# Kernel tuning notes

Hardware: AMD Instinct MI355X
Metric: run time of the kernel (lower is better)

## Reference

```python
import jax, jax.numpy as jnp
import numpy as np

HID, H, HKV, D, INT, S, T = 2048, 16, 8, 128, 6144, 4096, 512
POS = 0          # absolute position of the first token in this prefill chunk
EPS = 1e-6
SCALE = 1.0 / D ** 0.5
REP = H // HKV


def setup_inputs() -> dict:
    key = jax.random.key(0)
    ks = jax.random.split(key, 12)
    w = lambda k, sh: jax.random.normal(k, sh, dtype=jnp.float32) * 0.02

    hidden_conv = jax.random.normal(ks[0], (1, HID, 1, T), dtype=jnp.float32)

    # RoPE tables for absolute positions POS..POS+T-1, HF half-rotation layout
    inv_freq = 1.0 / (10000.0 ** (jnp.arange(0, D, 2, dtype=jnp.float32) / D))
    pos = (POS + jnp.arange(T, dtype=jnp.float32))
    ang = pos[:, None] * inv_freq[None, :]                      # (T, D/2)
    emb = jnp.concatenate([ang, ang], axis=-1)                  # (T, D)
    cos = jnp.cos(emb)[None]                                    # (1, T, D)
    sin = jnp.sin(emb)[None]

    # one-hot write mask: column t has a 1 at row POS+t
    update_mask = jnp.zeros((S, T), jnp.float32).at[POS + jnp.arange(T), jnp.arange(T)].set(1.0)[None, None]
    # causal mask over the cache: slot s visible to token t iff s <= POS+t
    attn_mask = jnp.where(jnp.arange(S)[None, :] <= (POS + jnp.arange(T))[:, None], 0.0, -1e4).astype(jnp.float32)[None, None]

    k_cache = jnp.zeros((1, HKV, S, D), jnp.float32)
    v_cache = jnp.zeros((1, HKV, S, D), jnp.float32)

    return dict(
        hidden_conv=hidden_conv, cos=cos, sin=sin,
        update_mask=update_mask, attn_mask=attn_mask,
        k_cache=k_cache, v_cache=v_cache,
        wq=w(ks[1], (H * D, HID)), wk=w(ks[2], (HKV * D, HID)),
        wv=w(ks[3], (HKV * D, HID)), wo=w(ks[4], (HID, H * D)),
        ln1_w=jnp.ones((HID,), jnp.float32), ln2_w=jnp.ones((HID,), jnp.float32),
        qn_w=jnp.ones((D,), jnp.float32), kn_w=jnp.ones((D,), jnp.float32),
        w_gate_up=w(ks[5], (2 * INT, HID)), w_down=w(ks[6], (HID, INT)),
    )


def _rms(x, w):
    return x * jax.lax.rsqrt(jnp.mean(x * x, axis=-1, keepdims=True) + EPS) * w


def _rotate_half(x):
    x1, x2 = jnp.split(x, 2, axis=-1)
    return jnp.concatenate([-x2, x1], axis=-1)


def reference(hidden_conv, cos, sin, update_mask, attn_mask, k_cache, v_cache,
              wq, wk, wv, wo, ln1_w, ln2_w, qn_w, kn_w, w_gate_up, w_down):
    # (1, HID, 1, T) conv layout -> (1, T, HID)
    x = jnp.transpose(hidden_conv[:, :, 0, :], (0, 2, 1))

    h = _rms(x, ln1_w)
    # 1x1 conv == linear; channel order h*D+d matches view(1,H,D,T)
    q = jnp.einsum('btc,oc->bto', h, wq).reshape(1, T, H, D).transpose(0, 2, 1, 3)    # (1,H,T,D)
    k = jnp.einsum('btc,oc->bto', h, wk).reshape(1, T, HKV, D).transpose(0, 2, 1, 3)  # (1,HKV,T,D)
    v = jnp.einsum('btc,oc->bto', h, wv).reshape(1, T, HKV, D).transpose(0, 2, 1, 3)

    q = _rms(q, qn_w)
    k = _rms(k, kn_w)

    cos_b = cos[:, None]  # (1,1,T,D)
    sin_b = sin[:, None]
    q = q * cos_b + _rotate_half(q) * sin_b
    k = k * cos_b + _rotate_half(k) * sin_b

    # matmul-based KV cache write via one-hot mask (faithful to original)
    k_inc = jnp.matmul(update_mask, k)                 # (1,HKV,S,D)
    v_inc = jnp.matmul(update_mask, v)
    write_any = jnp.sum(update_mask, axis=-1, keepdims=True)  # (1,1,S,1)
    k_full = k_cache * (1.0 - write_any) + k_inc
    v_full = v_cache * (1.0 - write_any) + v_inc

    k_rep = jnp.repeat(k_full, REP, axis=1)            # (1,H,S,D)
    v_rep = jnp.repeat(v_full, REP, axis=1)

    scores = jnp.einsum('bhtd,bhsd->bhts', q, k_rep) * SCALE + attn_mask  # (1,H,T,S)
    attn = jax.nn.softmax(scores, axis=-1)
    out = jnp.einsum('bhts,bhsd->bhtd', attn, v_rep)   # (1,H,T,D)

    o_in = out.transpose(0, 2, 1, 3).reshape(1, T, H * D)
    attn_out = jnp.einsum('btc,oc->bto', o_in, wo)
    hidden = x + attn_out

    h2 = _rms(hidden, ln2_w)
    gate_up = jnp.einsum('btc,oc->bto', h2, w_gate_up)
    gate, up = jnp.split(gate_up, 2, axis=-1)
    mlp = jnp.einsum('bti,oi->bto', jax.nn.silu(gate) * up, w_down)
    hidden = hidden + mlp

    hidden_out = jnp.transpose(hidden, (0, 2, 1))[:, :, None, :]  # back to (1,HID,1,T)
    return hidden_out, k_full, v_full


if __name__ == '__main__':
    outs = reference(**setup_inputs())
    print([o.shape for o in outs])
```

## Files before the change

### kernel.cpp

```cpp
#include <hip/hip_runtime.h>
#include <hip/hip_bf16.h>

#define TT 512
#define HIDD 2048
#define NH 16
#define NKV 8
#define DD 128
#define INTR 6144
#define SEQ 4096
#define SCALE 0.08838834764831845f

typedef __attribute__((ext_vector_type(8))) short short8;
typedef __attribute__((ext_vector_type(4))) float floatx4;

static __device__ __forceinline__ unsigned short f2b(float f) {
  unsigned int u = __float_as_uint(f);
  u += 0x7fffu + ((u >> 16) & 1u);
  return (unsigned short)(u >> 16);
}

static __device__ __forceinline__ unsigned int f2b2(float a, float b) {
  __hip_bfloat162 h = __float22bfloat162_rn(make_float2(a, b));
  return *reinterpret_cast<unsigned int*>(&h);
}


template <int BM, bool H> struct TR;
template <> struct TR<128, true>  { short8 v[2]; };
template <> struct TR<128, false> { float4 v[4]; };
template <> struct TR<64, true>   { short8 v[1]; };
template <> struct TR<64, false>  { float4 v[2]; };

template <int BM, bool H>
static __device__ __forceinline__ void tile_load(const void* __restrict__ src, int ld, int k0,
                                                 int tid, TR<BM, H>& r) {
  if constexpr (H) {
    const unsigned short* s = (const unsigned short*)src;
    const int r0 = tid >> 2, c8 = (tid & 3) << 3;
#pragma unroll
    for (int i = 0; i < BM / 64; ++i)
      r.v[i] = *reinterpret_cast<const short8*>(s + (size_t)(r0 + (i << 6)) * ld + k0 + c8);
  } else {
    const float* s = (const float*)src;
    const int r0 = tid >> 3, c4 = (tid & 7) << 2;
#pragma unroll
    for (int i = 0; i < BM / 32; ++i)
      r.v[i] = *reinterpret_cast<const float4*>(s + (size_t)(r0 + (i << 5)) * ld + k0 + c4);
  }
}

template <int BM, bool H>
static __device__ __forceinline__ void tile_store(const TR<BM, H>& r, unsigned short* dst, int tid) {
  if constexpr (H) {
    const int r0 = tid >> 2, c8 = (tid & 3) << 3;
#pragma unroll
    for (int i = 0; i < BM / 64; ++i)
      *reinterpret_cast<short8*>(dst + (r0 + (i << 6)) * 40 + c8) = r.v[i];
  } else {
    const int r0 = tid >> 3, c4 = (tid & 7) << 2;
#pragma unroll
    for (int i = 0; i < BM / 32; ++i) {
      uint2 o;
      o.x = f2b2(r.v[i].x, r.v[i].y);
      o.y = f2b2(r.v[i].z, r.v[i].w);
      *reinterpret_cast<uint2*>(dst + (r0 + (i << 5)) * 40 + c4) = o;
    }
  }
}

template <int BM, bool A16, bool B16>
static __device__ __forceinline__ void gemm_core(const void* __restrict__ A, int lda,
                                                 const void* __restrict__ B, int ldb,
                                                 int kbeg, int kend, floatx4 (&acc)[BM / 32][4],
                                                 unsigned short* As, unsigned short* Bs) {
  constexpr int MI = BM / 32;
  const int tid = threadIdx.x;
  const int lane = tid & 63;
  const int wave = tid >> 6;
  const int wr = (wave >> 1) * (BM >> 1);
  const int wc = (wave & 1) << 6;
  const int lrow = lane & 15;
  const int koff = (lane >> 4) << 3;
  TR<BM, A16> ra;
  TR<128, B16> rb;
  tile_load<BM, A16>(A, lda, kbeg, tid, ra);
  tile_load<128, B16>(B, ldb, kbeg, tid, rb);
  tile_store<BM, A16>(ra, As, tid);
  tile_store<128, B16>(rb, Bs, tid);
  if (kbeg + 32 < kend) {
    tile_load<BM, A16>(A, lda, kbeg + 32, tid, ra);
    tile_load<128, B16>(B, ldb, kbeg + 32, tid, rb);
  }
  __syncthreads();
  int p = 0;
  for (int k0 = kbeg; k0 < kend; k0 += 32) {
    const unsigned short* Ac = As + p * (BM * 40);
    const unsigned short* Bc = Bs + p * (128 * 40);
    unsigned short* An = As + (p ^ 1) * (BM * 40);
    unsigned short* Bn = Bs + (p ^ 1) * (128 * 40);
    short8 af[MI], bfr[4];
#pragma unroll
    for (int mi = 0; mi < MI; ++mi)
      af[mi] = *reinterpret_cast<const short8*>(Ac + (wr + mi * 16 + lrow) * 40 + koff);
#pragma unroll
    for (int ni = 0; ni < 4; ++ni)
      bfr[ni] = *reinterpret_cast<const short8*>(Bc + (wc + ni * 16 + lrow) * 40 + koff);
    if (k0 + 32 < kend) {
      tile_store<BM, A16>(ra, An, tid);
      tile_store<128, B16>(rb, Bn, tid);
      if (k0 + 64 < kend) {
        tile_load<BM, A16>(A, lda, k0 + 64, tid, ra);
        tile_load<128, B16>(B, ldb, k0 + 64, tid, rb);
      }
    }
#pragma unroll
    for (int mi = 0; mi < MI; ++mi)
#pragma unroll
      for (int ni = 0; ni < 4; ++ni)
        acc[mi][ni] = __builtin_amdgcn_mfma_f32_16x16x32_bf16(af[mi], bfr[ni], acc[mi][ni], 0, 0, 0);
    __syncthreads();
    p ^= 1;
  }
}

#define EPI_VARS \
  const int lane = threadIdx.x & 63; \
  const int wave = threadIdx.x >> 6; \
  const int wc = (wave & 1) << 6;    \
  const int lrow = lane & 15;        \
  const int quad = lane >> 4;

#define ZERO_ACC(MI_) \
  floatx4 acc[MI_][4]; \
  _Pragma("unroll") for (int mi = 0; mi < MI_; ++mi) \
  _Pragma("unroll") for (int ni = 0; ni < 4; ++ni) { floatx4 z = {0.f, 0.f, 0.f, 0.f}; acc[mi][ni] = z; }

template <int S>
static __device__ __forceinline__ void swz(int b, int& mt, int& nt, int& s) {
  mt = (b >> 3) & 3;
  const int gid = ((b >> 5) << 3) | (b & 7);
  nt = gid / S;
  s = gid - nt * S;
}


__global__ __launch_bounds__(1024) void k_rms1(const float* __restrict__ conv,
                                               const float* __restrict__ w,
                                               float* __restrict__ xb,
                                               unsigned short* __restrict__ h1b) {
  const int t0 = blockIdx.x << 5;
  const int tid = threadIdx.x;
  const int j = tid & 31;
  const int g = tid >> 5;
  __shared__ float part[32][32];
  __shared__ float tile[32][33];
  __shared__ float rs[32];
  float ss = 0.f;
  for (int c0 = 0; c0 < HIDD; c0 += 32) {
    const float v = conv[(size_t)(c0 + g) * TT + t0 + j];
    ss += v * v;
  }
  part[g][j] = ss;
  __syncthreads();
  if (g == 0) {
    float tot = 0.f;
#pragma unroll
    for (int q = 0; q < 32; ++q) tot += part[q][j];
    rs[j] = rsqrtf(tot * (1.0f / HIDD) + 1e-6f);
  }
  __syncthreads();
  for (int c0 = 0; c0 < HIDD; c0 += 32) {
    tile[g][j] = conv[(size_t)(c0 + g) * TT + t0 + j];
    __syncthreads();
    const float v = tile[j][g];
    const float rv = rs[g];
    xb[(size_t)(t0 + g) * HIDD + c0 + j] = v;
    h1b[(size_t)(t0 + g) * HIDD + c0 + j] = f2b(v * rv * w[c0 + j]);
    __syncthreads();
  }
}

__global__ __launch_bounds__(256) void k_gemm_qkv(const unsigned short* __restrict__ h1b,
                                                  const float* __restrict__ wq,
                                                  const float* __restrict__ wk,
                                                  const float* __restrict__ wv,
                                                  float* __restrict__ Pq) {
  __shared__ unsigned short As[2 * 128 * 40], Bs[2 * 128 * 40];
  int mt, nt, s;
  swz<4>(blockIdx.x, mt, nt, s);
  const int m0 = mt << 7, n0 = nt << 7;
  const float* Bp;
  if (n0 < 2048)      Bp = wq + (size_t)n0 * HIDD;
  else if (n0 < 3072) Bp = wk + (size_t)(n0 - 2048) * HIDD;
  else                Bp = wv + (size_t)(n0 - 3072) * HIDD;
  ZERO_ACC(4)
  gemm_core<128, true, false>(h1b + (size_t)m0 * HIDD, HIDD, Bp, HIDD, s * 512, s * 512 + 512, acc, As, Bs);
  EPI_VARS
  const int wr = (wave >> 1) << 6;
  float* out = Pq + (size_t)s * (TT * 4096);
#pragma unroll
  for (int mi = 0; mi < 4; ++mi)
#pragma unroll
    for (int ni = 0; ni < 4; ++ni)
#pragma unroll
      for (int rr = 0; rr < 4; ++rr) {
        const int row = m0 + wr + mi * 16 + quad * 4 + rr;
        const int col = n0 + wc + ni * 16 + lrow;
        out[(size_t)row * 4096 + col] = acc[mi][ni][rr];
      }
}

__global__ __launch_bounds__(128) void k_rope(const float* __restrict__ Pq,
                                              const float* __restrict__ cosb,
                                              const float* __restrict__ sinb,
                                              const float* __restrict__ qnw,
                                              const float* __restrict__ knw,
                                              unsigned short* __restrict__ qb,
                                              unsigned short* __restrict__ kb,
                                              unsigned short* __restrict__ vtb,
                                              float* __restrict__ kout,
                                              float* __restrict__ vout) {
  const int u = blockIdx.x;
  const int t = blockIdx.y;
  const int d = threadIdx.x;
  __shared__ float red[2];
  __shared__ float sh[DD];
  int slot;
  if (u < NH)            slot = u * DD + d;
  else if (u < NH + NKV) slot = 2048 + (u - NH) * DD + d;
  else                   slot = 3072 + (u - NH - NKV) * DD + d;
  const size_t idx = (size_t)t * 4096 + slot;
  float val = Pq[idx] + Pq[idx + TT * 4096] + Pq[idx + 2 * TT * 4096] + Pq[idx + 3 * TT * 4096];
  if (u < NH + NKV) {
    float ss = val * val;
    const int lane = d & 63, wid = d >> 6;
#pragma unroll
    for (int o = 32; o; o >>= 1) ss += __shfl_xor(ss, o);
    if (!lane) red[wid] = ss;
    __syncthreads();
    const float r = rsqrtf((red[0] + red[1]) * (1.0f / DD) + 1e-6f);
    const float w = (u < NH) ? qnw[d] : knw[d];
    const float nv = val * r * w;
    sh[d] = nv;
    __syncthreads();
    const float partner = sh[d ^ 64];
    const float rh = (d < 64) ? -partner : partner;
    const float o = nv * cosb[(size_t)t * DD + d] + rh * sinb[(size_t)t * DD + d];
    if (u < NH) {
      qb[(size_t)u * TT * DD + (size_t)t * DD + d] = f2b(o);
    } else {
      const int kh = u - NH;
      kout[(size_t)kh * SEQ * DD + (size_t)t * DD + d] = o;
      kb[(size_t)kh * TT * DD + (size_t)t * DD + d] = f2b(o);
    }
  } else {
    const int vh = u - NH - NKV;
    vout[(size_t)vh * SEQ * DD + (size_t)t * DD + d] = val;
    vtb[(size_t)vh * DD * TT + (size_t)d * TT + t] = f2b(val);
  }
}

__global__ __launch_bounds__(256) void k_tail(const float* __restrict__ kc,
                                              const float* __restrict__ vc,
                                              float* __restrict__ ko,
                                              float* __restrict__ vo) {
  const int i = blockIdx.x * 256 + threadIdx.x;
  const int e = i << 2;
  const int s = (e >> 7) & (SEQ - 1);
  if (s >= TT) {
    reinterpret_cast<float4*>(ko)[i] = reinterpret_cast<const float4*>(kc)[i];
    reinterpret_cast<float4*>(vo)[i] = reinterpret_cast<const float4*>(vc)[i];
  }
}

__global__ __launch_bounds__(256) void k_scores(const unsigned short* __restrict__ qb,
                                                const unsigned short* __restrict__ kb,
                                                float* __restrict__ sc) {
  __shared__ unsigned short As[2 * 64 * 40], Bs[2 * 128 * 40];
  const int m0 = blockIdx.x << 6, n0 = blockIdx.y << 7, h = blockIdx.z;
  ZERO_ACC(2)
  gemm_core<64, true, true>(qb + (size_t)h * TT * DD + (size_t)m0 * DD, DD,
                            kb + (size_t)(h >> 1) * TT * DD + (size_t)n0 * DD, DD, 0, DD, acc, As, Bs);
  EPI_VARS
  const int wr = (wave >> 1) << 5;
  float* out = sc + (size_t)h * TT * TT;
#pragma unroll
  for (int mi = 0; mi < 2; ++mi)
#pragma unroll
    for (int ni = 0; ni < 4; ++ni)
#pragma unroll
      for (int rr = 0; rr < 4; ++rr) {
        const int t = m0 + wr + mi * 16 + quad * 4 + rr;
        const int s = n0 + wc + ni * 16 + lrow;
        float v = acc[mi][ni][rr] * SCALE;
        if (s > t) v += -10000.0f;
        out[(size_t)t * TT + s] = v;
      }
}

__global__ __launch_bounds__(256) void k_softmax(const float* __restrict__ sc,
                                                 unsigned short* __restrict__ Pb) {
  const int h = blockIdx.x >> 9, t = blockIdx.x & 511;
  const int tid = threadIdx.x;
  const float* row = sc + ((size_t)h * TT + t) * TT;
  float v0 = row[tid], v1 = row[tid + 256];
  __shared__ float red[4];
  const int lane = tid & 63, wid = tid >> 6;
  float m = fmaxf(v0, v1);
#pragma unroll
  for (int o = 32; o; o >>= 1) m = fmaxf(m, __shfl_xor(m, o));
  if (!lane) red[wid] = m;
  __syncthreads();
  m = fmaxf(fmaxf(red[0], red[1]), fmaxf(red[2], red[3]));
  const float e0 = __expf(v0 - m), e1 = __expf(v1 - m);
  float s = e0 + e1;
  __syncthreads();
#pragma unroll
  for (int o = 32; o; o >>= 1) s += __shfl_xor(s, o);
  if (!lane) red[wid] = s;
  __syncthreads();
  const float inv = 1.0f / (red[0] + red[1] + red[2] + red[3]);
  unsigned short* orow = Pb + ((size_t)h * TT + t) * TT;
  orow[tid] = f2b(e0 * inv);
  orow[tid + 256] = f2b(e1 * inv);
}

__global__ __launch_bounds__(256) void k_pv(const unsigned short* __restrict__ Pb,
                                            const unsigned short* __restrict__ vtb,
                                            float* __restrict__ Ppv) {
  __shared__ unsigned short As[2 * 64 * 40], Bs[2 * 128 * 40];
  const int m0 = blockIdx.x << 6, h = blockIdx.y, s = blockIdx.z;
  ZERO_ACC(2)
  gemm_core<64, true, true>(Pb + (size_t)h * TT * TT + (size_t)m0 * TT, TT,
                            vtb + (size_t)(h >> 1) * DD * TT, TT, s * 128, s * 128 + 128, acc, As, Bs);
  EPI_VARS
  const int wr = (wave >> 1) << 5;
  float* out = Ppv + (size_t)s * (TT * HIDD);
#pragma unroll
  for (int mi = 0; mi < 2; ++mi)
#pragma unroll
    for (int ni = 0; ni < 4; ++ni)
#pragma unroll
      for (int rr = 0; rr < 4; ++rr) {
        const int row = m0 + wr + mi * 16 + quad * 4 + rr;
        const int col = wc + ni * 16 + lrow;
        out[(size_t)row * HIDD + h * DD + col] = acc[mi][ni][rr];
      }
}

__global__ __launch_bounds__(256) void k_red_pv(const float* __restrict__ Ppv,
                                                unsigned short* __restrict__ o_inb) {
  const int i = blockIdx.x * 256 + threadIdx.x;
  const float4* p = reinterpret_cast<const float4*>(Ppv);
  float4 a = p[i];
  const float4 b = p[i + 262144], c = p[i + 524288], d = p[i + 786432];
  a.x += b.x + c.x + d.x; a.y += b.y + c.y + d.y;
  a.z += b.z + c.z + d.z; a.w += b.w + c.w + d.w;
  uint2 o;
  o.x = f2b2(a.x, a.y);
  o.y = f2b2(a.z, a.w);
  *reinterpret_cast<uint2*>(o_inb + (size_t)i * 4) = o;
}

__global__ __launch_bounds__(256) void k_gemm_o(const unsigned short* __restrict__ o_inb,
                                                const float* __restrict__ wo,
                                                float* __restrict__ Po) {
  __shared__ unsigned short As[2 * 128 * 40], Bs[2 * 128 * 40];
  int mt, nt, s;
  swz<8>(blockIdx.x, mt, nt, s);
  const int m0 = mt << 7, n0 = nt << 7;
  ZERO_ACC(4)
  gemm_core<128, true, false>(o_inb + (size_t)m0 * HIDD, HIDD, wo + (size_t)n0 * HIDD, HIDD,
                              s * 256, s * 256 + 256, acc, As, Bs);
  EPI_VARS
  const int wr = (wave >> 1) << 6;
  float* out = Po + (size_t)s * (TT * HIDD);
#pragma unroll
  for (int mi = 0; mi < 4; ++mi)
#pragma unroll
    for (int ni = 0; ni < 4; ++ni)
#pragma unroll
      for (int rr = 0; rr < 4; ++rr) {
        const int row = m0 + wr + mi * 16 + quad * 4 + rr;
        const int col = n0 + wc + ni * 16 + lrow;
        out[(size_t)row * HIDD + col] = acc[mi][ni][rr];
      }
}

__global__ __launch_bounds__(256) void k_rms2(const float* __restrict__ xb,
                                              const float* __restrict__ Po,
                                              const float* __restrict__ w,
                                              float* __restrict__ hidden,
                                              unsigned short* __restrict__ h2b) {
  const int t = blockIdx.x;
  const int tid = threadIdx.x;
  float2 v[4];
  float ss = 0.f;
#pragma unroll
  for (int i = 0; i < 4; ++i) {
    const int c = (tid << 1) + (i << 9);
    const size_t idx = (size_t)t * HIDD + c;
    float2 a = *reinterpret_cast<const float2*>(xb + idx);
#pragma unroll
    for (int sp = 0; sp < 8; ++sp) {
      const float2 b = *reinterpret_cast<const float2*>(Po + idx + (size_t)sp * (TT * HIDD));
      a.x += b.x; a.y += b.y;
    }
    v[i] = a;
    ss += a.x * a.x + a.y * a.y;
  }
  __shared__ float red[4];
  const int lane = tid & 63, wid = tid >> 6;
#pragma unroll
  for (int o = 32; o; o >>= 1) ss += __shfl_xor(ss, o);
  if (!lane) red[wid] = ss;
  __syncthreads();
  const float tot = red[0] + red[1] + red[2] + red[3];
  const float r = rsqrtf(tot * (1.0f / HIDD) + 1e-6f);
#pragma unroll
  for (int i = 0; i < 4; ++i) {
    const int c = (tid << 1) + (i << 9);
    const size_t idx = (size_t)t * HIDD + c;
    *reinterpret_cast<float2*>(hidden + idx) = v[i];
    const float2 wv2 = *reinterpret_cast<const float2*>(w + c);
    *reinterpret_cast<unsigned int*>(h2b + idx) = f2b2(v[i].x * r * wv2.x, v[i].y * r * wv2.y);
  }
}

__global__ __launch_bounds__(256) void k_gemm_gu(const unsigned short* __restrict__ h2b,
                                                 const float* __restrict__ wgu,
                                                 float* __restrict__ gu) {
  __shared__ unsigned short As[2 * 64 * 40], Bs[2 * 128 * 40];
  const int bid = blockIdx.x;
  const int mt = bid / 96, nt = bid - mt * 96;
  const int m0 = mt << 6, n0 = nt << 7;
  ZERO_ACC(2)
  gemm_core<64, true, false>(h2b + (size_t)m0 * HIDD, HIDD, wgu + (size_t)n0 * HIDD, HIDD,
                             0, HIDD, acc, As, Bs);
  EPI_VARS
  const int wr = (wave >> 1) << 5;
#pragma unroll
  for (int mi = 0; mi < 2; ++mi)
#pragma unroll
    for (int ni = 0; ni < 4; ++ni)
#pragma unroll
      for (int rr = 0; rr < 4; ++rr) {
        const int row = m0 + wr + mi * 16 + quad * 4 + rr;
        const int col = n0 + wc + ni * 16 + lrow;
        gu[(size_t)row * (2 * INTR) + col] = acc[mi][ni][rr];
      }
}

__global__ __launch_bounds__(256) void k_silu(const float* __restrict__ gu,
                                              unsigned short* __restrict__ actb) {
  const int j0 = (blockIdx.x * 256 + threadIdx.x) << 1;
  const int t = blockIdx.y;
  const float2 g = *reinterpret_cast<const float2*>(gu + (size_t)t * (2 * INTR) + j0);
  const float2 u = *reinterpret_cast<const float2*>(gu + (size_t)t * (2 * INTR) + INTR + j0);
  const float a0 = g.x / (1.f + __expf(-g.x)) * u.x;
  const float a1 = g.y / (1.f + __expf(-g.y)) * u.y;
  *reinterpret_cast<unsigned int*>(actb + (size_t)t * INTR + j0) = f2b2(a0, a1);
}

__global__ __launch_bounds__(256) void k_gemm_down(const unsigned short* __restrict__ actb,
                                                   const float* __restrict__ wdn,
                                                   float* __restrict__ Pdn) {
  __shared__ unsigned short As[2 * 128 * 40], Bs[2 * 128 * 40];
  int mt, nt, s;
  swz<8>(blockIdx.x, mt, nt, s);
  const int m0 = mt << 7, n0 = nt << 7;
  ZERO_ACC(4)
  gemm_core<128, true, false>(actb + (size_t)m0 * INTR, INTR, wdn + (size_t)n0 * INTR, INTR,
                              s * 768, s * 768 + 768, acc, As, Bs);
  EPI_VARS
  const int wr = (wave >> 1) << 6;
  float* out = Pdn + (size_t)s * (TT * HIDD);
#pragma unroll
  for (int mi = 0; mi < 4; ++mi)
#pragma unroll
    for (int ni = 0; ni < 4; ++ni)
#pragma unroll
      for (int rr = 0; rr < 4; ++rr) {
        const int row = m0 + wr + mi * 16 + quad * 4 + rr;
        const int col = n0 + wc + ni * 16 + lrow;
        out[(size_t)row * HIDD + col] = acc[mi][ni][rr];
      }
}

__global__ __launch_bounds__(256) void k_final(const float* __restrict__ hidden,
                                               const float* __restrict__ Pdn,
                                               float* __restrict__ out0) {
  __shared__ float tile[32][33];
  const int c0 = blockIdx.x << 5, t0 = blockIdx.y << 5;
  const int tx = threadIdx.x & 31, ty0 = (threadIdx.x >> 5) << 2;
#pragma unroll
  for (int i = 0; i < 4; ++i) {
    const int t = t0 + ty0 + i;
    const size_t idx = (size_t)t * HIDD + c0 + tx;
    float a = hidden[idx];
#pragma unroll
    for (int sp = 0; sp < 8; ++sp) a += Pdn[idx + (size_t)sp * (TT * HIDD)];
    tile[ty0 + i][tx] = a;
  }
  __syncthreads();
#pragma unroll
  for (int i = 0; i < 4; ++i)
    out0[(size_t)(c0 + ty0 + i) * TT + t0 + tx] = tile[tx][ty0 + i];
}

extern "C" void kernel_launch(void* const* d_in, const int* in_sizes, int n_in,
                              void* d_out, int out_size, void* d_ws, size_t ws_size,
                              hipStream_t stream) {
  const float* conv   = (const float*)d_in[0];
  const float* cosb   = (const float*)d_in[1];
  const float* sinb   = (const float*)d_in[2];
  const float* kcache = (const float*)d_in[5];
  const float* vcache = (const float*)d_in[6];
  const float* wq  = (const float*)d_in[7];
  const float* wk  = (const float*)d_in[8];
  const float* wv  = (const float*)d_in[9];
  const float* wo  = (const float*)d_in[10];
  const float* ln1 = (const float*)d_in[11];
  const float* ln2 = (const float*)d_in[12];
  const float* qnw = (const float*)d_in[13];
  const float* knw = (const float*)d_in[14];
  const float* wgu = (const float*)d_in[15];
  const float* wdn = (const float*)d_in[16];

  float* ws = (float*)d_ws;
  float* xb = ws + 0;
  unsigned short* h1b  = (unsigned short*)(ws + 1048576);
  unsigned short* o_inb = h1b;
  unsigned short* h2b  = (unsigned short*)(ws + 1572864);
  float* hidden = ws + 2097152;
  unsigned short* qb  = (unsigned short*)(ws + 3145728);
  unsigned short* kb  = qb + 1048576;
  unsigned short* vtb = kb + 524288;
  unsigned short* actb = (unsigned short*)(ws + 4194304);
  float* R   = ws + 5767168;
  float* Pq  = R;
  unsigned short* Pb = (unsigned short*)R;
  float* sc  = R + 2097152;
  float* Ppv = R + 2097152;
  float* Po  = R;
  float* gu  = R;
  float* Pdn = R;

  float* out0 = (float*)d_out;
  float* kout = out0 + 1048576;
  float* vout = kout + 4194304;

  k_rms1<<<16, 1024, 0, stream>>>(conv, ln1, xb, h1b);
  k_gemm_qkv<<<512, 256, 0, stream>>>(h1b, wq, wk, wv, Pq);
  k_rope<<<dim3(NH + 2 * NKV, TT), 128, 0, stream>>>(Pq, cosb, sinb, qnw, knw, qb, kb, vtb, kout, vout);
  k_tail<<<4096, 256, 0, stream>>>(kcache, vcache, kout, vout);
  k_scores<<<dim3(8, 4, NH), 256, 0, stream>>>(qb, kb, sc);
  k_softmax<<<NH * TT, 256, 0, stream>>>(sc, Pb);
  k_pv<<<dim3(8, NH, 4), 256, 0, stream>>>(Pb, vtb, Ppv);
  k_red_pv<<<1024, 256, 0, stream>>>(Ppv, o_inb);
  k_gemm_o<<<512, 256, 0, stream>>>(o_inb, wo, Po);
  k_rms2<<<TT, 256, 0, stream>>>(xb, Po, ln2, hidden, h2b);
  k_gemm_gu<<<768, 256, 0, stream>>>(h2b, wgu, gu);
  k_silu<<<dim3(12, TT), 256, 0, stream>>>(gu, actb);
  k_gemm_down<<<512, 256, 0, stream>>>(actb, wdn, Pdn);
  k_final<<<dim3(HIDD / 32, TT / 32), 256, 0, stream>>>(hidden, Pdn, out0);
}
```

Baseline: 482.4 us.

## Load GEMM tiles straight into LDS with global_load_lds and XOR-swizzled layout

Replaces the register-staged, double-buffered GEMM mainloop with direct global-to-LDS loads (global_load_lds, 16 bytes per lane). The fp32 weight tile now stays fp32 in LDS and is converted to bf16 after the fragment read. Padded row strides are replaced by XOR swizzles to avoid bank conflicts. All GEMMs move to 64-row M tiles, and the launch grids for the qkv, o and down projections double to match. The intent is to cut VGPR pressure and register round-trips and to raise occupancy. In exchange, the loop is single-buffered with two barriers per K step and reads more LDS for the fp32 weights.

```diff
diff --git a/kernel.cpp b/kernel.cpp
--- a/kernel.cpp
+++ b/kernel.cpp
@@ -24,124 +24,115 @@
   return *reinterpret_cast<unsigned int*>(&h);
 }
 
-
-template <int BM, bool H> struct TR;
-template <> struct TR<128, true>  { short8 v[2]; };
-template <> struct TR<128, false> { float4 v[4]; };
-template <> struct TR<64, true>   { short8 v[1]; };
-template <> struct TR<64, false>  { float4 v[2]; };
-
-template <int BM, bool H>
-static __device__ __forceinline__ void tile_load(const void* __restrict__ src, int ld, int k0,
-                                                 int tid, TR<BM, H>& r) {
-  if constexpr (H) {
-    const unsigned short* s = (const unsigned short*)src;
-    const int r0 = tid >> 2, c8 = (tid & 3) << 3;
-#pragma unroll
-    for (int i = 0; i < BM / 64; ++i)
-      r.v[i] = *reinterpret_cast<const short8*>(s + (size_t)(r0 + (i << 6)) * ld + k0 + c8);
-  } else {
-    const float* s = (const float*)src;
-    const int r0 = tid >> 3, c4 = (tid & 7) << 2;
-#pragma unroll
-    for (int i = 0; i < BM / 32; ++i)
-      r.v[i] = *reinterpret_cast<const float4*>(s + (size_t)(r0 + (i << 5)) * ld + k0 + c4);
-  }
-}
-
-template <int BM, bool H>
-static __device__ __forceinline__ void tile_store(const TR<BM, H>& r, unsigned short* dst, int tid) {
-  if constexpr (H) {
-    const int r0 = tid >> 2, c8 = (tid & 3) << 3;
-#pragma unroll
-    for (int i = 0; i < BM / 64; ++i)
-      *reinterpret_cast<short8*>(dst + (r0 + (i << 6)) * 40 + c8) = r.v[i];
-  } else {
-    const int r0 = tid >> 3, c4 = (tid & 7) << 2;
-#pragma unroll
-    for (int i = 0; i < BM / 32; ++i) {
-      uint2 o;
-      o.x = f2b2(r.v[i].x, r.v[i].y);
-      o.y = f2b2(r.v[i].z, r.v[i].w);
-      *reinterpret_cast<uint2*>(dst + (r0 + (i << 5)) * 40 + c4) = o;
-    }
-  }
-}
-
-template <int BM, bool A16, bool B16>
-static __device__ __forceinline__ void gemm_core(const void* __restrict__ A, int lda,
-                                                 const void* __restrict__ B, int ldb,
-                                                 int kbeg, int kend, floatx4 (&acc)[BM / 32][4],
-                                                 unsigned short* As, unsigned short* Bs) {
-  constexpr int MI = BM / 32;
+static __device__ __forceinline__ void gl2lds(const void* g, void* l) {
+  __builtin_amdgcn_global_load_lds((const __attribute__((address_space(1))) void*)g,
+                                   (__attribute__((address_space(3))) void*)l, 16, 0, 0);
+}
+
+
+template <bool B16>
+static __device__ __forceinline__ void gemm_core64(const unsigned short* __restrict__ A, int lda,
+                                                   const void* __restrict__ B, int ldb,
+                                                   int kbeg, int kend, floatx4 (&acc)[2][4],
+                                                   unsigned short* As, void* Bs) {
   const int tid = threadIdx.x;
   const int lane = tid & 63;
   const int wave = tid >> 6;
-  const int wr = (wave >> 1) * (BM >> 1);
+  const int ar = tid >> 2, ac = tid & 3;
+  const unsigned short* aS = A + (size_t)ar * lda + ((ac ^ ((ar >> 1) & 3)) << 3) + kbeg;
+  const unsigned short* bS16[2];
+  const float* bS32[4];
+  if (B16) {
+    const unsigned short* Bh = (const unsigned short*)B;
+    const int swz = (tid & 3) ^ ((tid >> 3) & 3);
+#pragma unroll
+    for (int j = 0; j < 2; ++j)
+      bS16[j] = Bh + (size_t)((tid >> 2) + (j << 6)) * ldb + (swz << 3) + kbeg;
+  } else {
+    const float* Bf = (const float*)B;
+    const int swz = (tid & 7) ^ ((tid >> 3) & 7);
+#pragma unroll
+    for (int j = 0; j < 4; ++j)
+      bS32[j] = Bf + (size_t)((tid >> 3) + (j << 5)) * ldb + (swz << 2) + kbeg;
+  }
+  const int lrow = lane & 15, quad = lane >> 4;
+  const int wr = (wave >> 1) << 5;
   const int wc = (wave & 1) << 6;
-  const int lrow = lane & 15;
-  const int koff = (lane >> 4) << 3;
-  TR<BM, A16> ra;
-  TR<128, B16> rb;
-  tile_load<BM, A16>(A, lda, kbeg, tid, ra);
-  tile_load<128, B16>(B, ldb, kbeg, tid, rb);
-  tile_store<BM, A16>(ra, As, tid);
-  tile_store<128, B16>(rb, Bs, tid);
-  if (kbeg + 32 < kend) {
-    tile_load<BM, A16>(A, lda, kbeg + 32, tid, ra);
-    tile_load<128, B16>(B, ldb, kbeg + 32, tid, rb);
-  }
-  __syncthreads();
-  int p = 0;
+  const unsigned short* afp[2];
+#pragma unroll
+  for (int mi = 0; mi < 2; ++mi) {
+    const int r = wr + mi * 16 + lrow;
+    afp[mi] = As + r * 32 + ((quad ^ ((r >> 1) & 3)) << 3);
+  }
+  const unsigned short* bfp16[4];
+  const float* bfpa[4];
+  const float* bfpb[4];
+#pragma unroll
+  for (int ni = 0; ni < 4; ++ni) {
+    const int n = wc + ni * 16 + lrow;
+    if (B16) {
+      bfp16[ni] = (const unsigned short*)Bs + n * 32 + ((quad ^ ((n >> 1) & 3)) << 3);
+    } else {
+      const int c0 = (quad << 1) ^ (n & 7);
+      bfpa[ni] = (const float*)Bs + n * 32 + (c0 << 2);
+      bfpb[ni] = (const float*)Bs + n * 32 + ((c0 ^ 1) << 2);
+    }
+  }
   for (int k0 = kbeg; k0 < kend; k0 += 32) {
-    const unsigned short* Ac = As + p * (BM * 40);
-    const unsigned short* Bc = Bs + p * (128 * 40);
-    unsigned short* An = As + (p ^ 1) * (BM * 40);
-    unsigned short* Bn = Bs + (p ^ 1) * (128 * 40);
-    short8 af[MI], bfr[4];
-#pragma unroll
-    for (int mi = 0; mi < MI; ++mi)
-      af[mi] = *reinterpret_cast<const short8*>(Ac + (wr + mi * 16 + lrow) * 40 + koff);
-#pragma unroll
-    for (int ni = 0; ni < 4; ++ni)
-      bfr[ni] = *reinterpret_cast<const short8*>(Bc + (wc + ni * 16 + lrow) * 40 + koff);
-    if (k0 + 32 < kend) {
-      tile_store<BM, A16>(ra, An, tid);
-      tile_store<128, B16>(rb, Bn, tid);
-      if (k0 + 64 < kend) {
-        tile_load<BM, A16>(A, lda, k0 + 64, tid, ra);
-        tile_load<128, B16>(B, ldb, k0 + 64, tid, rb);
+    gl2lds(aS, As + (wave << 9));
+    aS += 32;
+    if (B16) {
+#pragma unroll
+      for (int j = 0; j < 2; ++j) {
+        gl2lds(bS16[j], (unsigned short*)Bs + (wave << 9) + (j << 11));
+        bS16[j] += 32;
+      }
+    } else {
+#pragma unroll
+      for (int j = 0; j < 4; ++j) {
+        gl2lds(bS32[j], (float*)Bs + (wave << 8) + (j << 10));
+        bS32[j] += 32;
       }
     }
-#pragma unroll
-    for (int mi = 0; mi < MI; ++mi)
+    __syncthreads();
+    short8 af[2], bfr[4];
+#pragma unroll
+    for (int mi = 0; mi < 2; ++mi) af[mi] = *reinterpret_cast<const short8*>(afp[mi]);
+    if (B16) {
+#pragma unroll
+      for (int ni = 0; ni < 4; ++ni) bfr[ni] = *reinterpret_cast<const short8*>(bfp16[ni]);
+    } else {
+#pragma unroll
+      for (int ni = 0; ni < 4; ++ni) {
+        const float4 fa = *reinterpret_cast<const float4*>(bfpa[ni]);
+        const float4 fb = *reinterpret_cast<const float4*>(bfpb[ni]);
+        uint4 u;
+        u.x = f2b2(fa.x, fa.y); u.y = f2b2(fa.z, fa.w);
+        u.z = f2b2(fb.x, fb.y); u.w = f2b2(fb.z, fb.w);
+        bfr[ni] = *reinterpret_cast<short8*>(&u);
+      }
+    }
+#pragma unroll
+    for (int mi = 0; mi < 2; ++mi)
 #pragma unroll
       for (int ni = 0; ni < 4; ++ni)
         acc[mi][ni] = __builtin_amdgcn_mfma_f32_16x16x32_bf16(af[mi], bfr[ni], acc[mi][ni], 0, 0, 0);
     __syncthreads();
-    p ^= 1;
   }
 }
 
 #define EPI_VARS \
   const int lane = threadIdx.x & 63; \
   const int wave = threadIdx.x >> 6; \
+  const int wr = (wave >> 1) << 5;   \
   const int wc = (wave & 1) << 6;    \
   const int lrow = lane & 15;        \
   const int quad = lane >> 4;
 
-#define ZERO_ACC(MI_) \
-  floatx4 acc[MI_][4]; \
-  _Pragma("unroll") for (int mi = 0; mi < MI_; ++mi) \
+#define ZERO_ACC \
+  floatx4 acc[2][4]; \
+  _Pragma("unroll") for (int mi = 0; mi < 2; ++mi) \
   _Pragma("unroll") for (int ni = 0; ni < 4; ++ni) { floatx4 z = {0.f, 0.f, 0.f, 0.f}; acc[mi][ni] = z; }
-
-template <int S>
-static __device__ __forceinline__ void swz(int b, int& mt, int& nt, int& s) {
-  mt = (b >> 3) & 3;
-  const int gid = ((b >> 5) << 3) | (b & 7);
-  nt = gid / S;
-  s = gid - nt * S;
-}
 
 
 __global__ __launch_bounds__(1024) void k_rms1(const float* __restrict__ conv,
@@ -185,21 +176,22 @@
                                                   const float* __restrict__ wk,
                                                   const float* __restrict__ wv,
                                                   float* __restrict__ Pq) {
-  __shared__ unsigned short As[2 * 128 * 40], Bs[2 * 128 * 40];
-  int mt, nt, s;
-  swz<4>(blockIdx.x, mt, nt, s);
-  const int m0 = mt << 7, n0 = nt << 7;
+  __shared__ unsigned short As[64 * 32];
+  __shared__ float Bsf[128 * 32];
+  const int bid = blockIdx.x;
+  const int mt = bid >> 7, gid = bid & 127;
+  const int nt = gid >> 2, s = gid & 3;
+  const int m0 = mt << 6, n0 = nt << 7;
   const float* Bp;
   if (n0 < 2048)      Bp = wq + (size_t)n0 * HIDD;
   else if (n0 < 3072) Bp = wk + (size_t)(n0 - 2048) * HIDD;
   else                Bp = wv + (size_t)(n0 - 3072) * HIDD;
-  ZERO_ACC(4)
-  gemm_core<128, true, false>(h1b + (size_t)m0 * HIDD, HIDD, Bp, HIDD, s * 512, s * 512 + 512, acc, As, Bs);
+  ZERO_ACC
+  gemm_core64<false>(h1b + (size_t)m0 * HIDD, HIDD, Bp, HIDD, s * 512, s * 512 + 512, acc, As, Bsf);
   EPI_VARS
-  const int wr = (wave >> 1) << 6;
   float* out = Pq + (size_t)s * (TT * 4096);
 #pragma unroll
-  for (int mi = 0; mi < 4; ++mi)
+  for (int mi = 0; mi < 2; ++mi)
 #pragma unroll
     for (int ni = 0; ni < 4; ++ni)
 #pragma unroll
@@ -276,13 +268,13 @@
 __global__ __launch_bounds__(256) void k_scores(const unsigned short* __restrict__ qb,
                                                 const unsigned short* __restrict__ kb,
                                                 float* __restrict__ sc) {
-  __shared__ unsigned short As[2 * 64 * 40], Bs[2 * 128 * 40];
+  __shared__ unsigned short As[64 * 32];
+  __shared__ unsigned short Bsh[128 * 32];
   const int m0 = blockIdx.x << 6, n0 = blockIdx.y << 7, h = blockIdx.z;
-  ZERO_ACC(2)
-  gemm_core<64, true, true>(qb + (size_t)h * TT * DD + (size_t)m0 * DD, DD,
-                            kb + (size_t)(h >> 1) * TT * DD + (size_t)n0 * DD, DD, 0, DD, acc, As, Bs);
+  ZERO_ACC
+  gemm_core64<true>(qb + (size_t)h * TT * DD + (size_t)m0 * DD, DD,
+                    kb + (size_t)(h >> 1) * TT * DD + (size_t)n0 * DD, DD, 0, DD, acc, As, Bsh);
   EPI_VARS
-  const int wr = (wave >> 1) << 5;
   float* out = sc + (size_t)h * TT * TT;
 #pragma unroll
   for (int mi = 0; mi < 2; ++mi)
@@ -328,13 +320,13 @@
 __global__ __launch_bounds__(256) void k_pv(const unsigned short* __restrict__ Pb,
                                             const unsigned short* __restrict__ vtb,
                                             float* __restrict__ Ppv) {
-  __shared__ unsigned short As[2 * 64 * 40], Bs[2 * 128 * 40];
+  __shared__ unsigned short As[64 * 32];
+  __shared__ unsigned short Bsh[128 * 32];
   const int m0 = blockIdx.x << 6, h = blockIdx.y, s = blockIdx.z;
-  ZERO_ACC(2)
-  gemm_core<64, true, true>(Pb + (size_t)h * TT * TT + (size_t)m0 * TT, TT,
-                            vtb + (size_t)(h >> 1) * DD * TT, TT, s * 128, s * 128 + 128, acc, As, Bs);
+  ZERO_ACC
+  gemm_core64<true>(Pb + (size_t)h * TT * TT + (size_t)m0 * TT, TT,
+                    vtb + (size_t)(h >> 1) * DD * TT, TT, s * 128, s * 128 + 128, acc, As, Bsh);
   EPI_VARS
-  const int wr = (wave >> 1) << 5;
   float* out = Ppv + (size_t)s * (TT * HIDD);
 #pragma unroll
   for (int mi = 0; mi < 2; ++mi)
@@ -365,18 +357,19 @@
 __global__ __launch_bounds__(256) void k_gemm_o(const unsigned short* __restrict__ o_inb,
                                                 const float* __restrict__ wo,
                                                 float* __restrict__ Po) {
-  __shared__ unsigned short As[2 * 128 * 40], Bs[2 * 128 * 40];
-  int mt, nt, s;
-  swz<8>(blockIdx.x, mt, nt, s);
-  const int m0 = mt << 7, n0 = nt << 7;
-  ZERO_ACC(4)
-  gemm_core<128, true, false>(o_inb + (size_t)m0 * HIDD, HIDD, wo + (size_t)n0 * HIDD, HIDD,
-                              s * 256, s * 256 + 256, acc, As, Bs);
+  __shared__ unsigned short As[64 * 32];
+  __shared__ float Bsf[128 * 32];
+  const int bid = blockIdx.x;
+  const int mt = bid >> 7, gid = bid & 127;
+  const int nt = gid >> 3, s = gid & 7;
+  const int m0 = mt << 6, n0 = nt << 7;
+  ZERO_ACC
+  gemm_core64<false>(o_inb + (size_t)m0 * HIDD, HIDD, wo + (size_t)n0 * HIDD, HIDD,
+                     s * 256, s * 256 + 256, acc, As, Bsf);
   EPI_VARS
-  const int wr = (wave >> 1) << 6;
   float* out = Po + (size_t)s * (TT * HIDD);
 #pragma unroll
-  for (int mi = 0; mi < 4; ++mi)
+  for (int mi = 0; mi < 2; ++mi)
 #pragma unroll
     for (int ni = 0; ni < 4; ++ni)
 #pragma unroll
@@ -430,15 +423,15 @@
 __global__ __launch_bounds__(256) void k_gemm_gu(const unsigned short* __restrict__ h2b,
                                                  const float* __restrict__ wgu,
                                                  float* __restrict__ gu) {
-  __shared__ unsigned short As[2 * 64 * 40], Bs[2 * 128 * 40];
+  __shared__ unsigned short As[64 * 32];
+  __shared__ float Bsf[128 * 32];
   const int bid = blockIdx.x;
   const int mt = bid / 96, nt = bid - mt * 96;
   const int m0 = mt << 6, n0 = nt << 7;
-  ZERO_ACC(2)
-  gemm_core<64, true, false>(h2b + (size_t)m0 * HIDD, HIDD, wgu + (size_t)n0 * HIDD, HIDD,
-                             0, HIDD, acc, As, Bs);
+  ZERO_ACC
+  gemm_core64<false>(h2b + (size_t)m0 * HIDD, HIDD, wgu + (size_t)n0 * HIDD, HIDD,
+                     0, HIDD, acc, As, Bsf);
   EPI_VARS
-  const int wr = (wave >> 1) << 5;
 #pragma unroll
   for (int mi = 0; mi < 2; ++mi)
 #pragma unroll
@@ -465,18 +458,19 @@
 __global__ __launch_bounds__(256) void k_gemm_down(const unsigned short* __restrict__ actb,
                                                    const float* __restrict__ wdn,
                                                    float* __restrict__ Pdn) {
-  __shared__ unsigned short As[2 * 128 * 40], Bs[2 * 128 * 40];
-  int mt, nt, s;
-  swz<8>(blockIdx.x, mt, nt, s);
-  const int m0 = mt << 7, n0 = nt << 7;
-  ZERO_ACC(4)
-  gemm_core<128, true, false>(actb + (size_t)m0 * INTR, INTR, wdn + (size_t)n0 * INTR, INTR,
-                              s * 768, s * 768 + 768, acc, As, Bs);
+  __shared__ unsigned short As[64 * 32];
+  __shared__ float Bsf[128 * 32];
+  const int bid = blockIdx.x;
+  const int mt = bid >> 7, gid = bid & 127;
+  const int nt = gid >> 3, s = gid & 7;
+  const int m0 = mt << 6, n0 = nt << 7;
+  ZERO_ACC
+  gemm_core64<false>(actb + (size_t)m0 * INTR, INTR, wdn + (size_t)n0 * INTR, INTR,
+                     s * 768, s * 768 + 768, acc, As, Bsf);
   EPI_VARS
-  const int wr = (wave >> 1) << 6;
   float* out = Pdn + (size_t)s * (TT * HIDD);
 #pragma unroll
-  for (int mi = 0; mi < 4; ++mi)
+  for (int mi = 0; mi < 2; ++mi)
 #pragma unroll
     for (int ni = 0; ni < 4; ++ni)
 #pragma unroll
@@ -551,17 +545,17 @@
   float* vout = kout + 4194304;
 
   k_rms1<<<16, 1024, 0, stream>>>(conv, ln1, xb, h1b);
-  k_gemm_qkv<<<512, 256, 0, stream>>>(h1b, wq, wk, wv, Pq);
+  k_gemm_qkv<<<1024, 256, 0, stream>>>(h1b, wq, wk, wv, Pq);
   k_rope<<<dim3(NH + 2 * NKV, TT), 128, 0, stream>>>(Pq, cosb, sinb, qnw, knw, qb, kb, vtb, kout, vout);
   k_tail<<<4096, 256, 0, stream>>>(kcache, vcache, kout, vout);
   k_scores<<<dim3(8, 4, NH), 256, 0, stream>>>(qb, kb, sc);
   k_softmax<<<NH * TT, 256, 0, stream>>>(sc, Pb);
   k_pv<<<dim3(8, NH, 4), 256, 0, stream>>>(Pb, vtb, Ppv);
   k_red_pv<<<1024, 256, 0, stream>>>(Ppv, o_inb);
-  k_gemm_o<<<512, 256, 0, stream>>>(o_inb, wo, Po);
+  k_gemm_o<<<1024, 256, 0, stream>>>(o_inb, wo, Po);
   k_rms2<<<TT, 256, 0, stream>>>(xb, Po, ln2, hidden, h2b);
   k_gemm_gu<<<768, 256, 0, stream>>>(h2b, wgu, gu);
   k_silu<<<dim3(12, TT), 256, 0, stream>>>(gu, actb);
-  k_gemm_down<<<512, 256, 0, stream>>>(actb, wdn, Pdn);
+  k_gemm_down<<<1024, 256, 0, stream>>>(actb, wdn, Pdn);
   k_final<<<dim3(HIDD / 32, TT / 32), 256, 0, stream>>>(hidden, Pdn, out0);
 }
```

New measurement: 493.7 us. 2.3% more time.
